# Kernel optimization log

Measured on AMD Instinct MI355X. Metric: run time of the kernel, lower is better.

The kernel has to match this reference:

```python
import jax, jax.numpy as jnp
import numpy as np

N_HEAD = 16

def setup_inputs() -> dict:
    key = jax.random.key(0)
    ks = jax.random.split(key, 6)
    C = 1024
    B, T, Tp = 8, 1024, 64
    s = 0.02
    return {
        "x": jax.random.normal(ks[0], (B, T, C), jnp.float32),
        "prefix_embd": jax.random.normal(ks[1], (B, Tp, C), jnp.float32),
        "w_attn": jax.random.normal(ks[2], (C, 3 * C), jnp.float32) * s,
        "b_attn": jnp.zeros((3 * C,), jnp.float32),
        "w_prefix": jax.random.normal(ks[3], (C, 3 * C), jnp.float32) * s,
        "b_prefix": jnp.zeros((3 * C,), jnp.float32),
        "w_proj": jax.random.normal(ks[4], (C, C), jnp.float32) * s,
        "b_proj": jnp.zeros((C,), jnp.float32),
    }

def _heads(t, H):
    B, T, C = t.shape
    return t.reshape(B, T, H, C // H).transpose(0, 2, 1, 3)  # (B,H,T,d)

def reference(x, prefix_embd, w_attn, b_attn, w_prefix, b_prefix, w_proj, b_proj):
    B, T, C = x.shape
    H = N_HEAD
    d = C // H
    Tp = prefix_embd.shape[1]
    scale = 1.0 / jnp.sqrt(jnp.asarray(d, x.dtype))

    qkv = x @ w_attn + b_attn
    q, k, v = (_heads(t, H) for t in jnp.split(qkv, 3, axis=2))  # (B,H,T,d)

    pqkv = prefix_embd @ w_prefix + b_prefix
    _, k_p, v_p = (_heads(t, H) for t in jnp.split(pqkv, 3, axis=2))  # (B,H,Tp,d)

    causal = jnp.tril(jnp.ones((T, T), bool))  # bias buffer slice
    neg_inf = jnp.asarray(float("-inf"), x.dtype)

    att = jnp.einsum("bhqd,bhkd->bhqk", q, k) * scale
    att = jnp.where(causal[None, None], att, neg_inf)
    att = jax.nn.softmax(att, axis=-1)

    att_p = jnp.einsum("bhqd,bhkd->bhqk", q, k_p) * scale
    att_p = jnp.where(causal[:, :Tp][None, None], att_p, neg_inf)
    att_p = jax.nn.softmax(att_p, axis=-1)

    y = jnp.einsum("bhqk,bhkd->bhqd", att_p, v_p) + jnp.einsum("bhqk,bhkd->bhqd", att, v)
    y = y.transpose(0, 2, 1, 3).reshape(B, T, C)
    return y @ w_proj + b_proj
```

## Files before the change

kernel.cpp:

```cpp
#include <hip/hip_runtime.h>
#include <hip/hip_bf16.h>
#include <cstdint>
#include <cstddef>

typedef __bf16 bf16_t;
typedef bf16_t bf16x8 __attribute__((ext_vector_type(8)));
typedef bf16_t bf16x4 __attribute__((ext_vector_type(4)));
typedef float f32x4 __attribute__((ext_vector_type(4)));

#define NB 8
#define NT 1024
#define NC 1024
#define NH 16
#define ND 64
#define NTP 64

__global__ __launch_bounds__(256) void k_cast2(const float* __restrict__ a, bf16_t* __restrict__ da,
                                               int n4a,
                                               const float* __restrict__ b2, bf16_t* __restrict__ db,
                                               int n4b) {
    int i = blockIdx.x * 256 + threadIdx.x;
    if (i < n4a) {
        float4 f = ((const float4*)a)[i];
        bf16x4 o;
        o[0] = (bf16_t)f.x; o[1] = (bf16_t)f.y; o[2] = (bf16_t)f.z; o[3] = (bf16_t)f.w;
        ((bf16x4*)da)[i] = o;
    } else {
        int j = i - n4a;
        if (j < n4b) {
            float4 f = ((const float4*)b2)[j];
            bf16x4 o;
            o[0] = (bf16_t)f.x; o[1] = (bf16_t)f.y; o[2] = (bf16_t)f.z; o[3] = (bf16_t)f.w;
            ((bf16x4*)db)[j] = o;
        }
    }
}

__global__ __launch_bounds__(256) void k_transpose3(const float* __restrict__ s0, bf16_t* __restrict__ d0,
                                                    const float* __restrict__ s1, bf16_t* __restrict__ d1,
                                                    const float* __restrict__ s2, bf16_t* __restrict__ d2) {
    __shared__ float tile[32][33];
    const int z = blockIdx.z;
    const float* src = (z == 0) ? s0 : (z == 1) ? s1 : s2;
    bf16_t* dst = (z == 0) ? d0 : (z == 1) ? d1 : d2;
    const int N = (z == 2) ? NC : 3 * NC;
    const int K = NC;
    if (z == 2 && blockIdx.x >= 32) return;
    int nt = blockIdx.x, kt = blockIdx.y;
    int tx = threadIdx.x & 31;
    int ty = threadIdx.x >> 5;
#pragma unroll
    for (int i = 0; i < 4; i++) {
        int r = ty + i * 8;
        tile[r][tx] = src[(size_t)(kt * 32 + r) * N + nt * 32 + tx];
    }
    __syncthreads();
#pragma unroll
    for (int i = 0; i < 4; i++) {
        int r = ty + i * 8;
        dst[(size_t)(nt * 32 + r) * K + kt * 32 + tx] = (bf16_t)tile[tx][r];
    }
}

__global__ __launch_bounds__(256) void k_gemm_qkv(const bf16_t* __restrict__ xb,
                                                  const bf16_t* __restrict__ pb,
                                                  const bf16_t* __restrict__ wTa,
                                                  const bf16_t* __restrict__ wTp,
                                                  const float* __restrict__ b_attn,
                                                  const float* __restrict__ b_prefix,
                                                  bf16_t* __restrict__ qkv,
                                                  bf16_t* __restrict__ pqkv) {
    const int bx = blockIdx.x;
    const int byw = blockIdx.y;
    const bool pre = (byw >= 64);
    const bf16_t* A = pre ? pb : xb;
    const bf16_t* BT = pre ? wTp : wTa;
    const float* bias = pre ? b_prefix : b_attn;
    bf16_t* Cout = pre ? pqkv : qkv;
    const int tsh = pre ? 6 : 10;
    const size_t rowA0 = (size_t)(pre ? (byw - 64) : byw) * 128;
    const size_t colB0 = (size_t)bx * 128;
    const int K = NC, N = 3 * NC;

    __shared__ bf16_t As[128 * 72];
    __shared__ bf16_t Bs[128 * 72];
    const int tid = threadIdx.x;
    const int lane = tid & 63;
    const int wave = tid >> 6;
    const int quad = lane >> 4;
    const int l15 = lane & 15;
    const int wm = (wave >> 1) * 64;
    const int wn = (wave & 1) * 64;

    const f32x4 fz = {0.f, 0.f, 0.f, 0.f};
    f32x4 acc[4][4];
#pragma unroll
    for (int i = 0; i < 4; i++)
#pragma unroll
        for (int j = 0; j < 4; j++) acc[i][j] = fz;

    for (int k0 = 0; k0 < K; k0 += 64) {
        __syncthreads();
#pragma unroll
        for (int i = 0; i < 4; i++) {
            int c = tid + i * 256;
            int r = c >> 3;
            int kc = (c & 7) * 8;
            uint4 av = *(const uint4*)(A + (rowA0 + r) * (size_t)K + k0 + kc);
            *(uint4*)(&As[r * 72 + kc]) = av;
            uint4 bv = *(const uint4*)(BT + (colB0 + r) * (size_t)K + k0 + kc);
            *(uint4*)(&Bs[r * 72 + kc]) = bv;
        }
        __syncthreads();
#pragma unroll
        for (int kk = 0; kk < 2; kk++) {
            bf16x8 af[4], bfr[4];
#pragma unroll
            for (int i = 0; i < 4; i++)
                af[i] = *(const bf16x8*)(&As[(wm + i * 16 + l15) * 72 + kk * 32 + quad * 8]);
#pragma unroll
            for (int j = 0; j < 4; j++)
                bfr[j] = *(const bf16x8*)(&Bs[(wn + j * 16 + l15) * 72 + kk * 32 + quad * 8]);
#pragma unroll
            for (int i = 0; i < 4; i++)
#pragma unroll
                for (int j = 0; j < 4; j++)
                    acc[i][j] = __builtin_amdgcn_mfma_f32_16x16x32_bf16(af[i], bfr[j], acc[i][j], 0, 0, 0);
        }
    }
    const bool vpath = (colB0 >= (size_t)(2 * NC));
#pragma unroll
    for (int i = 0; i < 4; i++) {
        size_t row = rowA0 + wm + i * 16 + quad * 4;
#pragma unroll
        for (int j = 0; j < 4; j++) {
            int col = (int)colB0 + wn + j * 16 + l15;
            float bv = bias[col];
            if (vpath) {
                int hh = (col - 2 * NC) >> 6;
                int dd = col & 63;
                int bb = (int)(row >> tsh);
                int tt = (int)row & ((1 << tsh) - 1);
                int tileBase = (bb * NH + hh) * (1 << (tsh - 6)) + (tt >> 6);
                size_t chunkrow = (size_t)tileBase * 4 + (dd >> 4);
                size_t addr = chunkrow * (size_t)N + 2 * NC + (dd & 15) * 64 + (tt & 63);
                bf16x4 vv;
#pragma unroll
                for (int r = 0; r < 4; r++) vv[r] = (bf16_t)(acc[i][j][r] + bv);
                *(bf16x4*)(Cout + addr) = vv;
            } else {
#pragma unroll
                for (int r = 0; r < 4; r++) {
                    float v = acc[i][j][r] + bv;
                    Cout[(row + r) * (size_t)N + col] = (bf16_t)v;
                }
            }
        }
    }
}

__global__ __launch_bounds__(256) void k_gemm_proj(const bf16_t* __restrict__ A,
                                                   const bf16_t* __restrict__ BT,
                                                   const float* __restrict__ bias,
                                                   float* __restrict__ Cout,
                                                   int M, int N, int K) {
    const int nwg = gridDim.x * gridDim.y;
    const int flat = blockIdx.y * gridDim.x + blockIdx.x;
    const int wgid = (flat & 7) * (nwg >> 3) + (flat >> 3);
    const int bx = wgid % gridDim.x;
    const int byw = wgid / gridDim.x;
    const size_t rowA0 = (size_t)byw * 128;
    const size_t colB0 = (size_t)bx * 128;

    __shared__ bf16_t As[128 * 72];
    __shared__ bf16_t Bs[128 * 72];
    const int tid = threadIdx.x;
    const int lane = tid & 63;
    const int wave = tid >> 6;
    const int quad = lane >> 4;
    const int l15 = lane & 15;
    const int wm = (wave >> 1) * 64;
    const int wn = (wave & 1) * 64;

    const f32x4 fz = {0.f, 0.f, 0.f, 0.f};
    f32x4 acc[4][4];
#pragma unroll
    for (int i = 0; i < 4; i++)
#pragma unroll
        for (int j = 0; j < 4; j++) acc[i][j] = fz;

    for (int k0 = 0; k0 < K; k0 += 64) {
        __syncthreads();
#pragma unroll
        for (int i = 0; i < 4; i++) {
            int c = tid + i * 256;
            int r = c >> 3;
            int kc = (c & 7) * 8;
            uint4 av = *(const uint4*)(A + (rowA0 + r) * (size_t)K + k0 + kc);
            *(uint4*)(&As[r * 72 + kc]) = av;
            uint4 bv = *(const uint4*)(BT + (colB0 + r) * (size_t)K + k0 + kc);
            *(uint4*)(&Bs[r * 72 + kc]) = bv;
        }
        __syncthreads();
#pragma unroll
        for (int kk = 0; kk < 2; kk++) {
            bf16x8 af[4], bfr[4];
#pragma unroll
            for (int i = 0; i < 4; i++)
                af[i] = *(const bf16x8*)(&As[(wm + i * 16 + l15) * 72 + kk * 32 + quad * 8]);
#pragma unroll
            for (int j = 0; j < 4; j++)
                bfr[j] = *(const bf16x8*)(&Bs[(wn + j * 16 + l15) * 72 + kk * 32 + quad * 8]);
#pragma unroll
            for (int i = 0; i < 4; i++)
#pragma unroll
                for (int j = 0; j < 4; j++)
                    acc[i][j] = __builtin_amdgcn_mfma_f32_16x16x32_bf16(af[i], bfr[j], acc[i][j], 0, 0, 0);
        }
    }
#pragma unroll
    for (int i = 0; i < 4; i++) {
        size_t row = rowA0 + wm + i * 16 + quad * 4;
#pragma unroll
        for (int j = 0; j < 4; j++) {
            int col = (int)colB0 + wn + j * 16 + l15;
            float bv = bias[col];
#pragma unroll
            for (int r = 0; r < 4; r++)
                Cout[(row + r) * (size_t)N + col] = acc[i][j][r] + bv;
        }
    }
}

#define LOADREGS(KB, VCB)                                                            \
    rk0 = *(const uint4*)((KB) + (size_t)(tid >> 3) * 3072 + (tid & 7) * 8);         \
    rv0 = *(const uint4*)((VCB) + (size_t)(tid >> 7) * 3072 + (tid & 127) * 8);

#define STAGE(KS, VS)                                                \
    *(uint4*)(&(KS)[(tid >> 3) * 72 + (tid & 7) * 8]) = rk0;         \
    *(uint4*)(&(VS)[(tid >> 3) * 72 + (tid & 7) * 8]) = rv0;

#define QK(KS, Sj, j)                                                                  \
    Sj = __builtin_amdgcn_mfma_f32_16x16x32_bf16(                                      \
        aq0, *(const bf16x8*)(&(KS)[((j) * 16 + l15) * 72 + quad * 8]), Sj, 0, 0, 0);  \
    Sj = __builtin_amdgcn_mfma_f32_16x16x32_bf16(                                      \
        aq1, *(const bf16x8*)(&(KS)[((j) * 16 + l15) * 72 + 32 + quad * 8]), Sj, 0, 0, 0);

#define EXPJ(Sj, j, BL, LACC)                                           \
    {                                                                   \
        const int n_ = (j) * 16 + l15;                                  \
        _Pragma("unroll") for (int r_ = 0; r_ < 4; r_++) {              \
            float p_ = __expf(Sj[r_] * scale);                          \
            if (n_ > (BL) + r_) p_ = 0.f;                               \
            Sj[r_] = p_;                                                \
            LACC[r_] += p_;                                             \
        }                                                               \
    }

#define PSTORE(Sj, j)                                                   \
    _Pragma("unroll") for (int r_ = 0; r_ < 4; r_++)                    \
        P[(quad * 4 + r_) * 72 + (j) * 16 + l15] = (bf16_t)Sj[r_];

#define PV(VS, Oj, j)                                                                  \
    Oj = __builtin_amdgcn_mfma_f32_16x16x32_bf16(                                      \
        ap0, *(const bf16x8*)(&(VS)[((j) * 16 + l15) * 72 + quad * 8]), Oj, 0, 0, 0);  \
    Oj = __builtin_amdgcn_mfma_f32_16x16x32_bf16(                                      \
        ap1, *(const bf16x8*)(&(VS)[((j) * 16 + l15) * 72 + 32 + quad * 8]), Oj, 0, 0, 0);

#define PROC(KS, VS, BL, LACC, O0, O1, O2, O3)                          \
    {                                                                   \
        f32x4 S0 = fz, S1 = fz, S2 = fz, S3 = fz;                       \
        __builtin_amdgcn_s_setprio(1);                                  \
        QK(KS, S0, 0) QK(KS, S1, 1) QK(KS, S2, 2) QK(KS, S3, 3)         \
        __builtin_amdgcn_s_setprio(0);                                  \
        EXPJ(S0, 0, BL, LACC) EXPJ(S1, 1, BL, LACC)                     \
        EXPJ(S2, 2, BL, LACC) EXPJ(S3, 3, BL, LACC)                     \
        PSTORE(S0, 0) PSTORE(S1, 1) PSTORE(S2, 2) PSTORE(S3, 3)         \
        __builtin_amdgcn_s_waitcnt(0xc07f);             \
        __builtin_amdgcn_wave_barrier();                                \
        bf16x8 ap0 = *(const bf16x8*)(&P[l15 * 72 + quad * 8]);         \
        bf16x8 ap1 = *(const bf16x8*)(&P[l15 * 72 + 32 + quad * 8]);    \
        __builtin_amdgcn_s_setprio(1);                                  \
        PV(VS, O0, 0) PV(VS, O1, 1) PV(VS, O2, 2) PV(VS, O3, 3)         \
        __builtin_amdgcn_s_setprio(0);                                  \
    }

#define STORE_O(Oj, Pj, j)                                                            \
    _Pragma("unroll") for (int r_ = 0; r_ < 4; r_++) {                                \
        float v_ = Oj[r_] * lmv[r_] + Pj[r_] * lpv[r_];                               \
        y[(qrow0 + quad * 4 + r_) * NC + h * 64 + (j) * 16 + l15] = (bf16_t)v_;       \
    }

__global__ __launch_bounds__(512, 2) void k_attn11(const bf16_t* __restrict__ qkv,
                                                   const bf16_t* __restrict__ pqkv,
                                                   bf16_t* __restrict__ y) {
    const int flat = (int)blockIdx.x + 8 * ((int)blockIdx.y + 16 * (int)blockIdx.z);
    const int wgid = (flat & 7) * 128 + (flat >> 3);
    const int qt = (NT / 128 - 1) - (wgid & 7);
    const int h = (wgid >> 3) & 15;
    const int b = wgid >> 7;
    const int TMAX = 2 * qt + 1;

    __shared__ bf16_t Ks0[64 * 72], Ks1[64 * 72];
    __shared__ bf16_t Vs0[64 * 72], Vs1[64 * 72];
    __shared__ bf16_t Ps[8][16 * 72];

    const int tid = threadIdx.x;
    const int lane = tid & 63;
    const int wave = tid >> 6;
    const int quad = lane >> 4;
    const int l15 = lane & 15;
    const float scale = 0.125f;

    const size_t qrow0 = (size_t)b * NT + (size_t)qt * 128 + wave * 16;
    const int qoff = qt * 128 + wave * 16 + quad * 4;
    bf16_t* P = Ps[wave];

    const bf16_t* Kmain = qkv + (size_t)(b * NT) * 3072 + NC + h * 64;
    const bf16_t* Vmain = qkv + (size_t)(b * NH + h) * 16 * 4 * 3072 + 2 * NC;
    const bf16_t* Vpre  = pqkv + (size_t)(b * NH + h) * 4 * 3072 + 2 * NC;

    bf16x8 aq0 = *(const bf16x8*)(qkv + (qrow0 + l15) * 3072 + h * 64 + quad * 8);
    bf16x8 aq1 = *(const bf16x8*)(qkv + (qrow0 + l15) * 3072 + h * 64 + 32 + quad * 8);

    const f32x4 fz = {0.f, 0.f, 0.f, 0.f};
    f32x4 Om0 = fz, Om1 = fz, Om2 = fz, Om3 = fz;
    f32x4 Op0 = fz, Op1 = fz, Op2 = fz, Op3 = fz;
    f32x4 Lm = fz, Lp = fz;
    uint4 rk0, rv0;

    LOADREGS(pqkv + (size_t)(b * NTP) * 3072 + NC + h * 64, Vpre)
    STAGE(Ks0, Vs0)
    LOADREGS(Kmain, Vmain)
    __syncthreads();
    PROC(Ks0, Vs0, qoff, Lp, Op0, Op1, Op2, Op3)
    STAGE(Ks1, Vs1)
    LOADREGS(Kmain + (size_t)64 * 3072, Vmain + 4 * 3072)

    for (int t = 0; t <= TMAX; t++) {
        __syncthreads();
        bf16_t* KSc = (t & 1) ? Ks0 : Ks1;
        bf16_t* VSc = (t & 1) ? Vs0 : Vs1;
        if (t < TMAX) {
            bf16_t* KSn = (t & 1) ? Ks1 : Ks0;
            bf16_t* VSn = (t & 1) ? Vs1 : Vs0;
            STAGE(KSn, VSn)
        }
        if (t + 1 < TMAX) {
            LOADREGS(Kmain + ((size_t)(t + 2) * 64) * 3072, Vmain + (size_t)(t + 2) * 4 * 3072)
        }
        PROC(KSc, VSc, qoff - t * 64, Lm, Om0, Om1, Om2, Om3)
    }

    f32x4 lmv, lpv;
#pragma unroll
    for (int r = 0; r < 4; r++) {
        float vm = Lm[r], vpr = Lp[r];
#pragma unroll
        for (int off = 1; off < 16; off <<= 1) {
            vm += __shfl_xor(vm, off, 64);
            vpr += __shfl_xor(vpr, off, 64);
        }
        lmv[r] = 1.0f / vm;
        lpv[r] = 1.0f / vpr;
    }

    STORE_O(Om0, Op0, 0) STORE_O(Om1, Op1, 1) STORE_O(Om2, Op2, 2) STORE_O(Om3, Op3, 3)
}

extern "C" void kernel_launch(void* const* d_in, const int* in_sizes, int n_in,
                              void* d_out, int out_size, void* d_ws, size_t ws_size,
                              hipStream_t stream) {
    (void)in_sizes; (void)n_in; (void)out_size; (void)ws_size;
    const float* x        = (const float*)d_in[0];
    const float* prefix   = (const float*)d_in[1];
    const float* w_attn   = (const float*)d_in[2];
    const float* b_attn   = (const float*)d_in[3];
    const float* w_prefix = (const float*)d_in[4];
    const float* b_prefix = (const float*)d_in[5];
    const float* w_proj   = (const float*)d_in[6];
    const float* b_proj   = (const float*)d_in[7];
    float* out = (float*)d_out;

    char* p = (char*)d_ws;
    auto carve = [&](size_t bytes) {
        char* q = p;
        p += (bytes + 255) & ~(size_t)255;
        return q;
    };
    bf16_t* xb   = (bf16_t*)carve((size_t)NB * NT * NC * 2);
    bf16_t* pb   = (bf16_t*)carve((size_t)NB * NTP * NC * 2);
    bf16_t* wTa  = (bf16_t*)carve((size_t)3 * NC * NC * 2);
    bf16_t* wTp  = (bf16_t*)carve((size_t)3 * NC * NC * 2);
    bf16_t* wTpr = (bf16_t*)carve((size_t)NC * NC * 2);
    bf16_t* qkv  = (bf16_t*)carve((size_t)NB * NT * 3 * NC * 2);
    bf16_t* pqkv = (bf16_t*)carve((size_t)NB * NTP * 3 * NC * 2);
    bf16_t* yb   = (bf16_t*)carve((size_t)NB * NT * NC * 2);

    const int n4a = NB * NT * NC / 4, n4b = NB * NTP * NC / 4;
    k_cast2<<<(n4a + n4b + 255) / 256, 256, 0, stream>>>(x, xb, n4a, prefix, pb, n4b);
    k_transpose3<<<dim3(3 * NC / 32, NC / 32, 3), 256, 0, stream>>>(w_attn, wTa, w_prefix, wTp,
                                                                    w_proj, wTpr);
    k_gemm_qkv<<<dim3(24, 68), 256, 0, stream>>>(xb, pb, wTa, wTp, b_attn, b_prefix, qkv, pqkv);
    k_attn11<<<dim3(NT / 128, NH, NB), 512, 0, stream>>>(qkv, pqkv, yb);
    k_gemm_proj<<<dim3(NC / 128, NB * NT / 128), 256, 0, stream>>>(
        yb, wTpr, b_proj, out, NB * NT, NC, NC);
}
```

Baseline: 300.5 us.

## Rewrite QKV GEMM with 256x256 tiles and async direct-to-LDS double buffering

Replaces the 128x128, 4-wave QKV projection GEMM with a 256x256-tile, 8-wave kernel. Operands are staged with global_load_lds straight into double-buffered LDS, and the next k-tile's A and B loads are interleaved between four MFMA phases. Those phases use explicit barriers, waitcnts and setprio. The goal is to hide global-load latency behind MFMA work and raise per-block data reuse. In exchange it needs 128KB of LDS per block, which limits occupancy. The unpadded LDS rows may cause read bank conflicts, and 408 blocks give an uneven final wave across the CUs.

After: 337.1 us. 12.2% more time.

```diff
diff --git a/kernel.cpp b/kernel.cpp
--- a/kernel.cpp
+++ b/kernel.cpp
@@ -62,7 +62,47 @@
     }
 }
 
-__global__ __launch_bounds__(256) void k_gemm_qkv(const bf16_t* __restrict__ xb,
+
+#define STG8(ldsptr, gptr)                                                                     \
+    {                                                                                          \
+        _Pragma("unroll") for (int i_ = 0; i_ < 2; i_++) {                                     \
+            const bf16_t* s_ =                                                                 \
+                (gptr) + (size_t)((wave * 2 + i_) * 8 + (lane >> 3)) * 1024 + (lane & 7) * 8;  \
+            __builtin_amdgcn_global_load_lds(                                                  \
+                (const __attribute__((address_space(1))) void*)s_,                             \
+                (__attribute__((address_space(3))) void*)((ldsptr) + (wave * 2 + i_) * 512),   \
+                16, 0, 0);                                                                     \
+        }                                                                                      \
+    }
+
+#define LDA8(mi_, kk_) (*(const bf16x8*)(&As[abase + ((mi_) * 16 + l15) * 64 + (kk_) * 32 + quad * 8]))
+#define LDB8(nj_, kk_) (*(const bf16x8*)(&Bs[bbase + (bloc + (nj_) * 16 + l15) * 64 + (kk_) * 32 + quad * 8]))
+
+#define PBAR()                               \
+    __builtin_amdgcn_sched_barrier(0);       \
+    __builtin_amdgcn_s_barrier();            \
+    __builtin_amdgcn_sched_barrier(0);
+
+#define LGKM0()                                        \
+    asm volatile("s_waitcnt lgkmcnt(0)" ::: "memory"); \
+    __builtin_amdgcn_sched_barrier(0);
+
+#define MFMAPH(c_)                                                                  \
+    __builtin_amdgcn_s_setprio(1);                                                  \
+    _Pragma("unroll") for (int m_ = 0; m_ < 2; m_++)                                \
+        _Pragma("unroll") for (int n_ = 0; n_ < 4; n_++) {                          \
+            acc[(c_) * 2 + m_][n_] = __builtin_amdgcn_mfma_f32_16x16x32_bf16(       \
+                af[m_ * 2 + 0], bfr[n_ * 2 + 0], acc[(c_) * 2 + m_][n_], 0, 0, 0);  \
+            acc[(c_) * 2 + m_][n_] = __builtin_amdgcn_mfma_f32_16x16x32_bf16(       \
+                af[m_ * 2 + 1], bfr[n_ * 2 + 1], acc[(c_) * 2 + m_][n_], 0, 0, 0);  \
+        }                                                                           \
+    __builtin_amdgcn_s_setprio(0);
+
+#define AFRD(base_)                                        \
+    af[0] = LDA8((base_) + 0, 0); af[1] = LDA8((base_) + 0, 1); \
+    af[2] = LDA8((base_) + 1, 0); af[3] = LDA8((base_) + 1, 1);
+
+__global__ __launch_bounds__(512, 2) void k_gemm8(const bf16_t* __restrict__ xb,
                                                   const bf16_t* __restrict__ pb,
                                                   const bf16_t* __restrict__ wTa,
                                                   const bf16_t* __restrict__ wTp,
@@ -72,65 +112,75 @@
                                                   bf16_t* __restrict__ pqkv) {
     const int bx = blockIdx.x;
     const int byw = blockIdx.y;
-    const bool pre = (byw >= 64);
+    const bool pre = (byw >= 32);
     const bf16_t* A = pre ? pb : xb;
     const bf16_t* BT = pre ? wTp : wTa;
     const float* bias = pre ? b_prefix : b_attn;
     bf16_t* Cout = pre ? pqkv : qkv;
     const int tsh = pre ? 6 : 10;
-    const size_t rowA0 = (size_t)(pre ? (byw - 64) : byw) * 128;
-    const size_t colB0 = (size_t)bx * 128;
-    const int K = NC, N = 3 * NC;
-
-    __shared__ bf16_t As[128 * 72];
-    __shared__ bf16_t Bs[128 * 72];
+    const size_t rowA0 = (size_t)(pre ? (byw - 32) : byw) * 256;
+    const size_t colB0 = (size_t)bx * 256;
+    const int N = 3 * NC;
+    const int NKT = 16;
+
+    __shared__ bf16_t As[2 * 2 * 128 * 64];
+    __shared__ bf16_t Bs[2 * 2 * 128 * 64];
+
     const int tid = threadIdx.x;
     const int lane = tid & 63;
     const int wave = tid >> 6;
     const int quad = lane >> 4;
     const int l15 = lane & 15;
-    const int wm = (wave >> 1) * 64;
-    const int wn = (wave & 1) * 64;
+    const int wm = (wave >> 2) * 128;
+    const int wn = (wave & 3) * 64;
+    const int ah = wm >> 7;
+    const int bh = wn >> 7;
+    const int bloc = wn & 127;
 
     const f32x4 fz = {0.f, 0.f, 0.f, 0.f};
-    f32x4 acc[4][4];
-#pragma unroll
-    for (int i = 0; i < 4; i++)
+    f32x4 acc[8][4];
+#pragma unroll
+    for (int i = 0; i < 8; i++)
 #pragma unroll
         for (int j = 0; j < 4; j++) acc[i][j] = fz;
-
-    for (int k0 = 0; k0 < K; k0 += 64) {
-        __syncthreads();
-#pragma unroll
-        for (int i = 0; i < 4; i++) {
-            int c = tid + i * 256;
-            int r = c >> 3;
-            int kc = (c & 7) * 8;
-            uint4 av = *(const uint4*)(A + (rowA0 + r) * (size_t)K + k0 + kc);
-            *(uint4*)(&As[r * 72 + kc]) = av;
-            uint4 bv = *(const uint4*)(BT + (colB0 + r) * (size_t)K + k0 + kc);
-            *(uint4*)(&Bs[r * 72 + kc]) = bv;
-        }
-        __syncthreads();
-#pragma unroll
-        for (int kk = 0; kk < 2; kk++) {
-            bf16x8 af[4], bfr[4];
-#pragma unroll
-            for (int i = 0; i < 4; i++)
-                af[i] = *(const bf16x8*)(&As[(wm + i * 16 + l15) * 72 + kk * 32 + quad * 8]);
-#pragma unroll
-            for (int j = 0; j < 4; j++)
-                bfr[j] = *(const bf16x8*)(&Bs[(wn + j * 16 + l15) * 72 + kk * 32 + quad * 8]);
-#pragma unroll
-            for (int i = 0; i < 4; i++)
-#pragma unroll
-                for (int j = 0; j < 4; j++)
-                    acc[i][j] = __builtin_amdgcn_mfma_f32_16x16x32_bf16(af[i], bfr[j], acc[i][j], 0, 0, 0);
-        }
-    }
+    bf16x8 af[4], bfr[8];
+
+    STG8(Bs + 0 * 8192, BT + colB0 * 1024)
+    STG8(Bs + 1 * 8192, BT + (colB0 + 128) * 1024)
+    STG8(As + 0 * 8192, A + rowA0 * 1024)
+    STG8(As + 1 * 8192, A + (rowA0 + 128) * 1024)
+    STG8(Bs + 2 * 8192, BT + colB0 * 1024 + 64)
+    STG8(Bs + 3 * 8192, BT + (colB0 + 128) * 1024 + 64)
+
+    for (int kt = 0; kt < NKT; kt++) {
+        const int cur = kt & 1, nxt = cur ^ 1;
+        const int abase = (cur * 2 + ah) * 8192;
+        const int bbase = (cur * 2 + bh) * 8192;
+        if (kt < NKT - 1) { asm volatile("s_waitcnt vmcnt(4)" ::: "memory"); }
+        else              { asm volatile("s_waitcnt vmcnt(0)" ::: "memory"); }
+        PBAR();
+        if (kt < NKT - 1) STG8(As + (nxt * 2 + 0) * 8192, A + rowA0 * 1024 + (kt + 1) * 64)
+#pragma unroll
+        for (int n_ = 0; n_ < 4; n_++) { bfr[n_ * 2] = LDB8(n_, 0); bfr[n_ * 2 + 1] = LDB8(n_, 1); }
+        AFRD(0)
+        LGKM0(); MFMAPH(0)
+        PBAR();
+        if (kt < NKT - 1) STG8(As + (nxt * 2 + 1) * 8192, A + (rowA0 + 128) * 1024 + (kt + 1) * 64)
+        AFRD(2)
+        LGKM0(); MFMAPH(1)
+        PBAR();
+        if (kt < NKT - 2) STG8(Bs + (cur * 2 + 0) * 8192, BT + colB0 * 1024 + (kt + 2) * 64)
+        AFRD(4)
+        LGKM0(); MFMAPH(2)
+        PBAR();
+        if (kt < NKT - 2) STG8(Bs + (cur * 2 + 1) * 8192, BT + (colB0 + 128) * 1024 + (kt + 2) * 64)
+        AFRD(6)
+        LGKM0(); MFMAPH(3)
+    }
+
     const bool vpath = (colB0 >= (size_t)(2 * NC));
 #pragma unroll
-    for (int i = 0; i < 4; i++) {
+    for (int i = 0; i < 8; i++) {
         size_t row = rowA0 + wm + i * 16 + quad * 4;
 #pragma unroll
         for (int j = 0; j < 4; j++) {
@@ -401,7 +451,7 @@
     k_cast2<<<(n4a + n4b + 255) / 256, 256, 0, stream>>>(x, xb, n4a, prefix, pb, n4b);
     k_transpose3<<<dim3(3 * NC / 32, NC / 32, 3), 256, 0, stream>>>(w_attn, wTa, w_prefix, wTp,
                                                                     w_proj, wTpr);
-    k_gemm_qkv<<<dim3(24, 68), 256, 0, stream>>>(xb, pb, wTa, wTp, b_attn, b_prefix, qkv, pqkv);
+    k_gemm8<<<dim3(12, 34), 512, 0, stream>>>(xb, pb, wTa, wTp, b_attn, b_prefix, qkv, pqkv);
     k_attn11<<<dim3(NT / 128, NH, NB), 512, 0, stream>>>(qkv, pqkv, yb);
     k_gemm_proj<<<dim3(NC / 128, NB * NT / 128), 256, 0, stream>>>(
         yb, wTpr, b_proj, out, NB * NT, NC, NC);
```
